# Kernel tuning notes

Measured on AMD Instinct MI355X. Metric: run time of the kernel, lower is better.

The kernel has to match this reference:

```python
import jax, jax.numpy as jnp
import numpy as np


def setup_inputs() -> dict:
    key = jax.random.key(0)
    ks = jax.random.split(key, 12)
    B, N, E = 8, 10000, 320000
    x = jax.random.normal(ks[0], (B, N, 3), dtype=jnp.float32)
    edge_index = jax.random.randint(ks[1], (2, E), 0, N, dtype=jnp.int64)
    # edge_attr: [dist, direction]; dist kept away from 0 to avoid div-by-zero
    dist = jax.random.uniform(ks[2], (E,), dtype=jnp.float32) * 9.0 + 1.0
    direc = jax.random.uniform(ks[3], (E,), dtype=jnp.float32) * 2.0 * np.pi
    edge_attr = jnp.stack([dist, direc], axis=-1)
    wind_mean = jax.random.uniform(ks[4], (2,), dtype=jnp.float32) * 2.0
    wind_std = jax.random.uniform(ks[5], (2,), dtype=jnp.float32) + 0.5
    s = lambda k, sh, fan: jax.random.normal(k, sh, dtype=jnp.float32) / np.sqrt(fan)
    W1 = s(ks[6], (9, 16), 9)
    b1 = jnp.zeros((16,), jnp.float32)
    W2 = s(ks[7], (16, 30), 16)
    b2 = jnp.zeros((30,), jnp.float32)
    W3 = s(ks[8], (30, 3), 30)
    b3 = jnp.zeros((3,), jnp.float32)
    return {"x": x, "edge_index": edge_index, "edge_attr": edge_attr,
            "wind_mean": wind_mean, "wind_std": wind_std,
            "W1": W1, "b1": b1, "W2": W2, "b2": b2, "W3": W3, "b3": b3}


def reference(x, edge_index, edge_attr, wind_mean, wind_std, W1, b1, W2, b2, W3, b3):
    B, N, _ = x.shape
    src, tgt = edge_index[0], edge_index[1]
    node_src = x[:, src]    # [B,E,3] gather
    node_tgt = x[:, tgt]    # [B,E,3]
    # denormalize wind (last 2 features of source node)
    src_wind = node_src[:, :, -2:] * wind_std[None, None, :] + wind_mean[None, None, :]
    speed = src_wind[:, :, 0]
    direc = src_wind[:, :, 1]
    city_dist = edge_attr[:, 0][None, :]   # [1,E]
    city_direc = edge_attr[:, 1][None, :]
    theta = jnp.abs(city_direc - direc)
    edge_weight = jax.nn.relu(3.0 * speed * jnp.cos(theta) / city_dist)  # [B,E]
    # normalize edge_attr (torch .std uses ddof=1)
    ea_norm = (edge_attr - edge_attr.mean(axis=0)) / edge_attr.std(axis=0, ddof=1)
    ea_norm_b = jnp.broadcast_to(ea_norm[None], (B,) + ea_norm.shape)
    feat = jnp.concatenate([node_src, node_tgt, ea_norm_b, edge_weight[:, :, None]], axis=-1)  # [B,E,9]
    h = jax.nn.sigmoid(feat @ W1 + b1)
    h = jax.nn.sigmoid(h @ W2 + b2)        # [B,E,30]
    agg = jnp.zeros((B, N, h.shape[-1]), h.dtype)
    agg = agg.at[:, tgt].add(h).at[:, src].add(-h)   # scatter_add + scatter_sub
    return jax.nn.sigmoid(agg @ W3 + b3)   # [B,N,3]
```

## Files before the change

kernel.cpp:

```cpp
#include <hip/hip_runtime.h>
#include <hip/hip_fp16.h>
#include <math.h>

#define BB 8
#define NB 128
#define NBINS 10016
#define FPAD 14

typedef float f32x2 __attribute__((ext_vector_type(2)));
typedef float f32x4 __attribute__((ext_vector_type(4)));
typedef _Float16 h16x4 __attribute__((ext_vector_type(4)));

__device__ __forceinline__ float sigmoidf_(float v) {
    return __builtin_amdgcn_rcpf(1.0f + __expf(-v));
}
__device__ __forceinline__ float sigs_(float d) {
    return __builtin_amdgcn_rcpf(1.0f + __builtin_amdgcn_exp2f(-d));
}
__device__ __forceinline__ unsigned pkh2_(float a, float b) {
    __half2 h = __floats2half2_rn(a, b);
    return *reinterpret_cast<unsigned*>(&h);
}

__global__ __launch_bounds__(256) void prep_kernel(
    const float* __restrict__ ea, const int* __restrict__ ei,
    const float* __restrict__ x, float* __restrict__ xT,
    unsigned short* __restrict__ cnt2, double* __restrict__ acc,
    int N, int E, int full)
{
    __shared__ unsigned hist[NBINS];
    __shared__ double sh[4][256];
    int tid = threadIdx.x;
    int blk = blockIdx.x;

    if (full) {
        for (int b = tid; b < NBINS; b += 256) hist[b] = 0u;
    }

    double s0 = 0, q0 = 0, s1 = 0, q1 = 0;
    for (int i = blk * 256 + tid; i < E; i += NB * 256) {
        float a = ea[2 * i];
        float b = ea[2 * i + 1];
        s0 += (double)a; q0 += (double)a * (double)a;
        s1 += (double)b; q1 += (double)b * (double)b;
    }

    if (full) {
        int xtotal = N * BB * 3;
        for (int idx = blk * 256 + tid; idx < xtotal; idx += NB * 256) {
            int c = idx % 3;
            int rest = idx / 3;
            int n = rest % N;
            int b = rest / N;
            xT[n * 24 + b * 3 + c] = x[idx];
        }
        __syncthreads();
        int chunk = (E + NB - 1) / NB;
        int s = blk * chunk;
        int epd = min(E, s + chunk);
        for (int e = s + tid; e < epd; e += 256) {
            atomicAdd(&hist[ei[E + e]], 1u);
            atomicAdd(&hist[ei[e]], 1u);
        }
        __syncthreads();
        unsigned short* row = cnt2 + (size_t)blk * NBINS;
        for (int b = tid; b < NBINS; b += 256)
            row[b] = (unsigned short)hist[b];
    }

    sh[0][tid] = s0; sh[1][tid] = q0; sh[2][tid] = s1; sh[3][tid] = q1;
    __syncthreads();
    for (int off = 128; off > 0; off >>= 1) {
        if (tid < off) {
            sh[0][tid] += sh[0][tid + off];
            sh[1][tid] += sh[1][tid + off];
            sh[2][tid] += sh[2][tid + off];
            sh[3][tid] += sh[3][tid + off];
        }
        __syncthreads();
    }
    if (tid == 0) {
        atomicAdd(&acc[0], sh[0][0]);
        atomicAdd(&acc[1], sh[1][0]);
        atomicAdd(&acc[2], sh[2][0]);
        atomicAdd(&acc[3], sh[3][0]);
    }
}

__global__ __launch_bounds__(256) void base_kernel(unsigned short* __restrict__ cnt2,
                                                   int* __restrict__ tot) {
    int bin = blockIdx.x * 256 + threadIdx.x;
    if (bin >= NBINS) return;
    unsigned run = 0;
    #pragma unroll 8
    for (int blk = 0; blk < NB; blk++) {
        size_t idx = (size_t)blk * NBINS + bin;
        unsigned v = cnt2[idx];
        cnt2[idx] = (unsigned short)run;
        run += v;
    }
    tot[bin] = (int)run;
}

__global__ __launch_bounds__(1024) void scan_kernel(const int* __restrict__ tot,
                                                    int* __restrict__ off, int N,
                                                    const double* __restrict__ acc, int E,
                                                    float* __restrict__ stats) {
    if (threadIdx.x == 0) {
        double s0 = acc[0], q0 = acc[1], s1 = acc[2], q1 = acc[3];
        double v0 = (q0 - s0 * s0 / E) / (double)(E - 1);
        double v1 = (q1 - s1 * s1 / E) / (double)(E - 1);
        stats[0] = (float)(s0 / E);
        stats[1] = (float)(1.0 / sqrt(v0));
        stats[2] = (float)(s1 / E);
        stats[3] = (float)(1.0 / sqrt(v1));
    }
    __shared__ int sh[1024];
    int t = threadIdx.x;
    int chunk = (N + 1023) >> 10;
    int lo = t * chunk;
    int hi = lo + chunk; if (hi > N) hi = N;
    int s = 0;
    for (int i = lo; i < hi; i++) s += tot[i];
    sh[t] = s;
    __syncthreads();
    for (int d = 1; d < 1024; d <<= 1) {
        int v = (t >= d) ? sh[t - d] : 0;
        __syncthreads();
        sh[t] += v;
        __syncthreads();
    }
    int run = (t == 0) ? 0 : sh[t - 1];
    for (int i = lo; i < hi; i++) {
        off[i] = run;
        run += tot[i];
    }
    if (t == 1023) off[N] = sh[1023];
}

__global__ __launch_bounds__(256) void ranklist_kernel(
    const int* __restrict__ ei, int E,
    const unsigned short* __restrict__ cnt2,
    const int* __restrict__ off, int* __restrict__ list)
{
    __shared__ unsigned hist[NBINS];
    int tid = threadIdx.x;
    int blk = blockIdx.x;
    for (int b = tid; b < NBINS; b += 256) hist[b] = 0u;
    __syncthreads();

    int chunk = (E + NB - 1) / NB;
    int s = blk * chunk;
    int epd = min(E, s + chunk);
    const unsigned short* row = cnt2 + (size_t)blk * NBINS;
    for (int e = s + tid; e < epd; e += 256) {
        int tgt = ei[E + e];
        int src = ei[e];
        unsigned lt = atomicAdd(&hist[tgt], 1u);
        unsigned ls = atomicAdd(&hist[src], 1u);
        list[off[tgt] + (int)row[tgt] + (int)lt] = e;
        list[off[src] + (int)row[src] + (int)ls] = e | 0x80000000;
    }
}

__global__ __launch_bounds__(256) void edge_mlp_mfma_kernel(
    const float* __restrict__ xT, const int* __restrict__ ei,
    const float* __restrict__ ea,
    const float* __restrict__ wmean, const float* __restrict__ wstd,
    const float* __restrict__ W1, const float* __restrict__ b1,
    const float* __restrict__ W2, const float* __restrict__ b2,
    const float* __restrict__ W3,
    const double* __restrict__ acc,
    uint2* __restrict__ gbuf,
    int N, int E)
{
    __shared__ unsigned fsh[4][64][FPAD];

    int lane = threadIdx.x & 63;
    int wave = threadIdx.x >> 6;
    int g = lane >> 4;
    int arow = lane & 15;

    const float LOG2E = 1.44269504088896340736f;

    double as0 = acc[0], aq0 = acc[1], as1 = acc[2], aq1 = acc[3];
    double v0 = (aq0 - as0 * as0 / E) / (double)(E - 1);
    double v1 = (aq1 - as1 * as1 / E) / (double)(E - 1);
    float st0 = (float)(as0 / E);
    float st1 = (float)(1.0 / sqrt(v0));
    float st2 = (float)(as1 / E);
    float st3 = (float)(1.0 / sqrt(v1));

    h16x4 A1, A2a, A2b, A3a, A3b;
    #pragma unroll
    for (int j = 0; j < 4; j++) {
        int k = 4 * g + j;
        A1[j]  = (_Float16)((k < 9) ? W1[k * 16 + arow] * LOG2E : 0.0f);
        A2a[j] = (_Float16)(W2[k * 30 + arow] * LOG2E);
        A2b[j] = (_Float16)((arow < 14) ? W2[k * 30 + 16 + arow] * LOG2E : 0.0f);
        A3a[j] = (_Float16)((arow < 3) ? W3[k * 3 + arow] : 0.0f);
        int k2 = 16 + k;
        A3b[j] = (_Float16)((arow < 3 && k2 < 30) ? W3[k2 * 3 + arow] : 0.0f);
    }
    f32x4 C1, C2a, C2b;
    #pragma unroll
    for (int r = 0; r < 4; r++) {
        int row = 4 * g + r;
        C1[r]  = b1[row] * LOG2E;
        C2a[r] = b2[row] * LOG2E;
        C2b[r] = (row < 14) ? b2[16 + row] * LOG2E : 0.0f;
    }

    float wm0 = wmean[0], wm1 = wmean[1];
    float wsd0 = wstd[0], wsd1 = wstd[1];

    int e_loc = lane >> 3;
    int bb = lane & 7;

    for (int grp = blockIdx.x; grp * 32 < E; grp += gridDim.x) {
        int ebase = grp * 32 + wave * 8;
        if (ebase >= E) continue;

        int e = ebase + e_loc;
        int esafe = (e < E) ? e : (E - 1);
        int src = ei[esafe];
        int tgt = ei[E + esafe];
        float dist = ea[2 * esafe];
        float cdir = ea[2 * esafe + 1];

        const float* xs = xT + src * 24 + bb * 3;
        const float* xt = xT + tgt * 24 + bb * 3;
        float s0 = xs[0], s1 = xs[1], s2 = xs[2];
        float t0 = xt[0], t1 = xt[1], t2 = xt[2];
        float ea0 = (dist - st0) * st1;
        float ea1 = (cdir - st2) * st3;
        float speed = fmaf(s1, wsd0, wm0);
        float direc = fmaf(s2, wsd1, wm1);
        float theta = fabsf(cdir - direc);
        float ew = fmaxf(0.0f, speed * __cosf(theta) * 3.0f * __builtin_amdgcn_rcpf(dist));

        unsigned* fp = &fsh[wave][lane][0];
        uint4 wv0, wv1;
        wv0.x = pkh2_(s0, s1); wv0.y = pkh2_(s2, t0);
        wv0.z = pkh2_(t1, t2); wv0.w = pkh2_(ea0, ea1);
        wv1.x = pkh2_(ew, 0.0f); wv1.y = 0u; wv1.z = 0u; wv1.w = 0u;
        *reinterpret_cast<uint4*>(fp) = wv0;
        *reinterpret_cast<uint4*>(fp + 4) = wv1;

        #pragma unroll
        for (int t = 0; t < 4; t++) {
            const unsigned* q = &fsh[wave][t * 16 + arow][0];
            union { uint2 u; h16x4 h; } b1u;
            b1u.u = *reinterpret_cast<const uint2*>(q + 2 * g);

            f32x4 D1 = __builtin_amdgcn_mfma_f32_16x16x16f16(A1, b1u.h, C1, 0, 0, 0);
            union { uint2 u; h16x4 h; } b2u;
            b2u.u.x = pkh2_(sigs_(D1[0]), sigs_(D1[1]));
            b2u.u.y = pkh2_(sigs_(D1[2]), sigs_(D1[3]));

            f32x4 D2a = __builtin_amdgcn_mfma_f32_16x16x16f16(A2a, b2u.h, C2a, 0, 0, 0);
            f32x4 D2b = __builtin_amdgcn_mfma_f32_16x16x16f16(A2b, b2u.h, C2b, 0, 0, 0);
            union { uint2 u; h16x4 h; } b3au, b3bu;
            b3au.u.x = pkh2_(sigs_(D2a[0]), sigs_(D2a[1]));
            b3au.u.y = pkh2_(sigs_(D2a[2]), sigs_(D2a[3]));
            b3bu.u.x = pkh2_(sigs_(D2b[0]), sigs_(D2b[1]));
            b3bu.u.y = pkh2_(sigs_(D2b[2]), sigs_(D2b[3]));

            f32x4 Z = {0.f, 0.f, 0.f, 0.f};
            f32x4 D3 = __builtin_amdgcn_mfma_f32_16x16x16f16(A3a, b3au.h, Z, 0, 0, 0);
            D3 = __builtin_amdgcn_mfma_f32_16x16x16f16(A3b, b3bu.h, D3, 0, 0, 0);

            if (g == 0) {
                int et = ebase + 2 * t + (arow >> 3);
                int bt = arow & 7;
                if (et < E) {
                    uint2 wp;
                    wp.x = pkh2_(D3[0], D3[1]);
                    wp.y = pkh2_(D3[2], 0.0f);
                    gbuf[(size_t)et * BB + bt] = wp;
                }
            }
        }
    }
}

__global__ __launch_bounds__(256) void node_sum_kernel(
    const uint2* __restrict__ gbuf, const int* __restrict__ off,
    const int* __restrict__ list,
    const float* __restrict__ b3, float* __restrict__ out, int N)
{
    int node = blockIdx.x * 4 + (threadIdx.x >> 6);
    int lane = threadIdx.x & 63;
    if (node >= N) return;

    int o0 = off[node], o1 = off[node + 1];
    float a[BB][3];
    #pragma unroll
    for (int b = 0; b < BB; b++) { a[b][0] = 0.f; a[b][1] = 0.f; a[b][2] = 0.f; }

    for (int i = o0 + lane; i < o1; i += 64) {
        int entry = list[i];
        int e = entry & 0x7FFFFFFF;
        float sgn = (entry < 0) ? -1.0f : 1.0f;
        const uint4* gl = reinterpret_cast<const uint4*>(gbuf + (size_t)e * BB);
        uint4 q0 = gl[0], q1 = gl[1], q2 = gl[2], q3 = gl[3];

        #define ACC_(bi, u01, u2x) {                                              \
            float2 f01 = __half22float2(*reinterpret_cast<const __half2*>(&u01)); \
            float2 f2  = __half22float2(*reinterpret_cast<const __half2*>(&u2x)); \
            a[bi][0] = fmaf(sgn, f01.x, a[bi][0]);                                \
            a[bi][1] = fmaf(sgn, f01.y, a[bi][1]);                                \
            a[bi][2] = fmaf(sgn, f2.x,  a[bi][2]); }
        ACC_(0, q0.x, q0.y) ACC_(1, q0.z, q0.w)
        ACC_(2, q1.x, q1.y) ACC_(3, q1.z, q1.w)
        ACC_(4, q2.x, q2.y) ACC_(5, q2.z, q2.w)
        ACC_(6, q3.x, q3.y) ACC_(7, q3.z, q3.w)
        #undef ACC_
    }

    #pragma unroll
    for (int m = 32; m >= 1; m >>= 1) {
        #pragma unroll
        for (int b = 0; b < BB; b++) {
            a[b][0] += __shfl_xor(a[b][0], m);
            a[b][1] += __shfl_xor(a[b][1], m);
            a[b][2] += __shfl_xor(a[b][2], m);
        }
    }

    float bb0 = b3[0], bb1 = b3[1], bb2 = b3[2];
    #pragma unroll
    for (int b = 0; b < BB; b++) {
        if (lane == b) {
            float* o = out + ((size_t)b * N + node) * 3;
            o[0] = sigmoidf_(a[b][0] + bb0);
            o[1] = sigmoidf_(a[b][1] + bb1);
            o[2] = sigmoidf_(a[b][2] + bb2);
        }
    }
}

__global__ void finalize_stats_kernel(const double* __restrict__ acc, int E,
                                      float* __restrict__ stats) {
    double s0 = acc[0], q0 = acc[1], s1 = acc[2], q1 = acc[3];
    double v0 = (q0 - s0 * s0 / E) / (double)(E - 1);
    double v1 = (q1 - s1 * s1 / E) / (double)(E - 1);
    stats[0] = (float)(s0 / E);
    stats[1] = (float)(1.0 / sqrt(v0));
    stats[2] = (float)(s1 / E);
    stats[3] = (float)(1.0 / sqrt(v1));
}

__device__ __forceinline__ void mlp_eval(
    const float feat[9],
    const float* __restrict__ W1, const float* __restrict__ b1,
    const float* __restrict__ W2, const float* __restrict__ b2,
    const float* __restrict__ W3,
    float& g0, float& g1, float& g2)
{
    const f32x2* W1p = (const f32x2*)W1;
    const f32x2* b1p = (const f32x2*)b1;
    f32x2 acc1[8];
    #pragma unroll
    for (int j = 0; j < 8; j++) acc1[j] = b1p[j];
    #pragma unroll
    for (int k = 0; k < 9; k++) {
        f32x2 fk2 = {feat[k], feat[k]};
        #pragma unroll
        for (int j = 0; j < 8; j++)
            acc1[j] = __builtin_elementwise_fma(fk2, W1p[k * 8 + j], acc1[j]);
    }
    float h1[16];
    #pragma unroll
    for (int j = 0; j < 8; j++) {
        h1[2 * j]     = sigmoidf_(acc1[j].x);
        h1[2 * j + 1] = sigmoidf_(acc1[j].y);
    }
    const f32x2* W2p = (const f32x2*)W2;
    const f32x2* b2p = (const f32x2*)b2;
    f32x2 acc2[15];
    #pragma unroll
    for (int k = 0; k < 15; k++) acc2[k] = b2p[k];
    #pragma unroll
    for (int j = 0; j < 16; j++) {
        f32x2 hj2 = {h1[j], h1[j]};
        #pragma unroll
        for (int k = 0; k < 15; k++)
            acc2[k] = __builtin_elementwise_fma(hj2, W2p[j * 15 + k], acc2[k]);
    }
    g0 = 0.f; g1 = 0.f; g2 = 0.f;
    #pragma unroll
    for (int k = 0; k < 15; k++) {
        float ha = sigmoidf_(acc2[k].x);
        float hb = sigmoidf_(acc2[k].y);
        int ka = 2 * k, kb = 2 * k + 1;
        g0 = fmaf(ha, W3[ka * 3 + 0], g0); g0 = fmaf(hb, W3[kb * 3 + 0], g0);
        g1 = fmaf(ha, W3[ka * 3 + 1], g1); g1 = fmaf(hb, W3[kb * 3 + 1], g1);
        g2 = fmaf(ha, W3[ka * 3 + 2], g2); g2 = fmaf(hb, W3[kb * 3 + 2], g2);
    }
}

__global__ __launch_bounds__(256) void edge_atomic_kernel(
    const float* __restrict__ x, const int* __restrict__ ei,
    const float* __restrict__ ea,
    const float* __restrict__ wmean, const float* __restrict__ wstd,
    const float* __restrict__ W1, const float* __restrict__ b1,
    const float* __restrict__ W2, const float* __restrict__ b2,
    const float* __restrict__ W3,
    const float* __restrict__ stats,
    float* __restrict__ out, int N, int E)
{
    int e = blockIdx.x * blockDim.x + threadIdx.x;
    if (e >= E) return;
    int src = ei[e];
    int tgt = ei[E + e];
    float dist = ea[2 * e];
    float cdir = ea[2 * e + 1];
    float ea0 = (dist - stats[0]) * stats[1];
    float ea1 = (cdir - stats[2]) * stats[3];

    for (int b = 0; b < BB; b++) {
        const float* xb = x + (size_t)b * N * 3;
        float s0 = xb[src * 3 + 0], s1 = xb[src * 3 + 1], s2 = xb[src * 3 + 2];
        float t0 = xb[tgt * 3 + 0], t1 = xb[tgt * 3 + 1], t2 = xb[tgt * 3 + 2];
        float speed = fmaf(s1, wstd[0], wmean[0]);
        float direc = fmaf(s2, wstd[1], wmean[1]);
        float theta = fabsf(cdir - direc);
        float ew = fmaxf(0.0f, speed * __cosf(theta) * 3.0f * __builtin_amdgcn_rcpf(dist));
        float feat[9] = {s0, s1, s2, t0, t1, t2, ea0, ea1, ew};
        float g0, g1, g2;
        mlp_eval(feat, W1, b1, W2, b2, W3, g0, g1, g2);
        float* ot = out + ((size_t)b * N + tgt) * 3;
        float* os = out + ((size_t)b * N + src) * 3;
        atomicAdd(&ot[0], g0);  atomicAdd(&ot[1], g1);  atomicAdd(&ot[2], g2);
        atomicAdd(&os[0], -g0); atomicAdd(&os[1], -g1); atomicAdd(&os[2], -g2);
    }
}

__global__ void output_kernel(float* __restrict__ out, const float* __restrict__ b3, int total) {
    int i = blockIdx.x * blockDim.x + threadIdx.x;
    if (i < total) out[i] = sigmoidf_(out[i] + b3[i % 3]);
}

extern "C" void kernel_launch(void* const* d_in, const int* in_sizes, int n_in,
                              void* d_out, int out_size, void* d_ws, size_t ws_size,
                              hipStream_t stream) {
    const float* x     = (const float*)d_in[0];
    const int*   ei    = (const int*)d_in[1];
    const float* ea    = (const float*)d_in[2];
    const float* wmean = (const float*)d_in[3];
    const float* wstd  = (const float*)d_in[4];
    const float* W1    = (const float*)d_in[5];
    const float* b1    = (const float*)d_in[6];
    const float* W2    = (const float*)d_in[7];
    const float* b2    = (const float*)d_in[8];
    const float* W3    = (const float*)d_in[9];
    const float* b3    = (const float*)d_in[10];

    int E = in_sizes[2] / 2;
    int N = in_sizes[0] / (BB * 3);

    float* out = (float*)d_out;
    char* ws = (char*)d_ws;

    double* acc   = (double*)ws;
    float*  stats = (float*)(ws + 32);
    int*    tot   = (int*)(ws + 64);
    int*    off   = tot + NBINS;
    int*    list  = off + N + 1;

    size_t xtOff = 64 + sizeof(int) * ((size_t)NBINS + (N + 1) + 2 * (size_t)E);
    xtOff = (xtOff + 255) & ~(size_t)255;
    float* xT = (float*)(ws + xtOff);

    size_t c2Off = xtOff + (size_t)N * 24 * sizeof(float);
    c2Off = (c2Off + 255) & ~(size_t)255;
    unsigned short* cnt2 = (unsigned short*)(ws + c2Off);

    size_t gbOff = c2Off + (size_t)NB * NBINS * sizeof(unsigned short);
    gbOff = (gbOff + 255) & ~(size_t)255;
    uint2* gbuf = (uint2*)(ws + gbOff);
    size_t needed = gbOff + (size_t)E * BB * sizeof(uint2);

    int eblocks = (E + 255) / 256;
    int fastPath = (needed <= ws_size && N <= NBINS) ? 1 : 0;

    hipMemsetAsync(acc, 0, 32, stream);

    if (fastPath) {
        prep_kernel<<<NB, 256, 0, stream>>>(ea, ei, x, xT, cnt2, acc, N, E, 1);
        base_kernel<<<(NBINS + 255) / 256, 256, 0, stream>>>(cnt2, tot);
        scan_kernel<<<1, 1024, 0, stream>>>(tot, off, N, acc, E, stats);
        ranklist_kernel<<<NB, 256, 0, stream>>>(ei, E, cnt2, off, list);
        int groups = (E + 31) / 32;
        int mblocks = (groups < 2048) ? groups : 2048;
        edge_mlp_mfma_kernel<<<mblocks, 256, 0, stream>>>(
            xT, ei, ea, wmean, wstd, W1, b1, W2, b2, W3, acc, gbuf, N, E);
        node_sum_kernel<<<(N + 3) / 4, 256, 0, stream>>>(
            gbuf, off, list, b3, out, N);
    } else {
        hipMemsetAsync(d_out, 0, (size_t)out_size * sizeof(float), stream);
        prep_kernel<<<NB, 256, 0, stream>>>(ea, ei, x, xT, cnt2, acc, N, E, 0);
        finalize_stats_kernel<<<1, 1, 0, stream>>>(acc, E, stats);
        edge_atomic_kernel<<<eblocks, 256, 0, stream>>>(
            x, ei, ea, wmean, wstd, W1, b1, W2, b2, W3, stats, out, N, E);
        output_kernel<<<(out_size + 255) / 256, 256, 0, stream>>>(out, b3, out_size);
    }
}
```

Baseline: 120.6 us.

## Fuse ranklist into edge MLP kernel and replace stats atomics with per-block partials

```diff
diff --git a/kernel.cpp b/kernel.cpp
--- a/kernel.cpp
+++ b/kernel.cpp
@@ -25,7 +25,7 @@
 __global__ __launch_bounds__(256) void prep_kernel(
     const float* __restrict__ ea, const int* __restrict__ ei,
     const float* __restrict__ x, float* __restrict__ xT,
-    unsigned short* __restrict__ cnt2, double* __restrict__ acc,
+    unsigned short* __restrict__ cnt2, double* __restrict__ accp,
     int N, int E, int full)
 {
     __shared__ unsigned hist[NBINS];
@@ -80,10 +80,10 @@
         __syncthreads();
     }
     if (tid == 0) {
-        atomicAdd(&acc[0], sh[0][0]);
-        atomicAdd(&acc[1], sh[1][0]);
-        atomicAdd(&acc[2], sh[2][0]);
-        atomicAdd(&acc[3], sh[3][0]);
+        accp[4 * blk + 0] = sh[0][0];
+        accp[4 * blk + 1] = sh[1][0];
+        accp[4 * blk + 2] = sh[2][0];
+        accp[4 * blk + 3] = sh[3][0];
     }
 }
 
@@ -104,10 +104,16 @@
 
 __global__ __launch_bounds__(1024) void scan_kernel(const int* __restrict__ tot,
                                                     int* __restrict__ off, int N,
-                                                    const double* __restrict__ acc, int E,
+                                                    const double* __restrict__ accp, int E,
                                                     float* __restrict__ stats) {
     if (threadIdx.x == 0) {
-        double s0 = acc[0], q0 = acc[1], s1 = acc[2], q1 = acc[3];
+        double s0 = 0, q0 = 0, s1 = 0, q1 = 0;
+        for (int b = 0; b < NB; b++) {
+            s0 += accp[4 * b + 0];
+            q0 += accp[4 * b + 1];
+            s1 += accp[4 * b + 2];
+            q1 += accp[4 * b + 3];
+        }
         double v0 = (q0 - s0 * s0 / E) / (double)(E - 1);
         double v1 = (q1 - s1 * s1 / E) / (double)(E - 1);
         stats[0] = (float)(s0 / E);
@@ -138,58 +144,55 @@
     if (t == 1023) off[N] = sh[1023];
 }
 
-__global__ __launch_bounds__(256) void ranklist_kernel(
-    const int* __restrict__ ei, int E,
-    const unsigned short* __restrict__ cnt2,
-    const int* __restrict__ off, int* __restrict__ list)
-{
-    __shared__ unsigned hist[NBINS];
-    int tid = threadIdx.x;
-    int blk = blockIdx.x;
-    for (int b = tid; b < NBINS; b += 256) hist[b] = 0u;
-    __syncthreads();
-
-    int chunk = (E + NB - 1) / NB;
-    int s = blk * chunk;
-    int epd = min(E, s + chunk);
-    const unsigned short* row = cnt2 + (size_t)blk * NBINS;
-    for (int e = s + tid; e < epd; e += 256) {
-        int tgt = ei[E + e];
-        int src = ei[e];
-        unsigned lt = atomicAdd(&hist[tgt], 1u);
-        unsigned ls = atomicAdd(&hist[src], 1u);
-        list[off[tgt] + (int)row[tgt] + (int)lt] = e;
-        list[off[src] + (int)row[src] + (int)ls] = e | 0x80000000;
-    }
-}
-
-__global__ __launch_bounds__(256) void edge_mlp_mfma_kernel(
+__global__ __launch_bounds__(256) void fused_rank_mlp_kernel(
     const float* __restrict__ xT, const int* __restrict__ ei,
     const float* __restrict__ ea,
     const float* __restrict__ wmean, const float* __restrict__ wstd,
     const float* __restrict__ W1, const float* __restrict__ b1,
     const float* __restrict__ W2, const float* __restrict__ b2,
     const float* __restrict__ W3,
-    const double* __restrict__ acc,
+    const float* __restrict__ stats,
+    const unsigned short* __restrict__ cnt2,
+    const int* __restrict__ off, int* __restrict__ list,
     uint2* __restrict__ gbuf,
     int N, int E)
 {
-    __shared__ unsigned fsh[4][64][FPAD];
-
-    int lane = threadIdx.x & 63;
-    int wave = threadIdx.x >> 6;
+    __shared__ unsigned smem[NBINS];
+    int tid = threadIdx.x;
+
+    if (blockIdx.x < NB) {
+        unsigned* hist = smem;
+        int blk = blockIdx.x;
+        for (int b = tid; b < NBINS; b += 256) hist[b] = 0u;
+        __syncthreads();
+        int chunk = (E + NB - 1) / NB;
+        int s = blk * chunk;
+        int epd = min(E, s + chunk);
+        const unsigned short* row = cnt2 + (size_t)blk * NBINS;
+        for (int e = s + tid; e < epd; e += 256) {
+            int tgt = ei[E + e];
+            int src = ei[e];
+            unsigned lt = atomicAdd(&hist[tgt], 1u);
+            unsigned ls = atomicAdd(&hist[src], 1u);
+            list[off[tgt] + (int)row[tgt] + (int)lt] = e;
+            list[off[src] + (int)row[src] + (int)ls] = e | 0x80000000;
+        }
+        return;
+    }
+
+    typedef unsigned fsh_t[64][FPAD];
+    fsh_t* fsh = reinterpret_cast<fsh_t*>(smem);
+
+    int mlp_id = blockIdx.x - NB;
+    int nmlp = gridDim.x - NB;
+    int lane = tid & 63;
+    int wave = tid >> 6;
     int g = lane >> 4;
     int arow = lane & 15;
 
     const float LOG2E = 1.44269504088896340736f;
 
-    double as0 = acc[0], aq0 = acc[1], as1 = acc[2], aq1 = acc[3];
-    double v0 = (aq0 - as0 * as0 / E) / (double)(E - 1);
-    double v1 = (aq1 - as1 * as1 / E) / (double)(E - 1);
-    float st0 = (float)(as0 / E);
-    float st1 = (float)(1.0 / sqrt(v0));
-    float st2 = (float)(as1 / E);
-    float st3 = (float)(1.0 / sqrt(v1));
+    float st0 = stats[0], st1 = stats[1], st2 = stats[2], st3 = stats[3];
 
     h16x4 A1, A2a, A2b, A3a, A3b;
     #pragma unroll
@@ -217,7 +220,7 @@
     int e_loc = lane >> 3;
     int bb = lane & 7;
 
-    for (int grp = blockIdx.x; grp * 32 < E; grp += gridDim.x) {
+    for (int grp = mlp_id; grp * 32 < E; grp += nmlp) {
         int ebase = grp * 32 + wave * 8;
         if (ebase >= E) continue;
 
@@ -340,9 +343,15 @@
     }
 }
 
-__global__ void finalize_stats_kernel(const double* __restrict__ acc, int E,
+__global__ void finalize_stats_kernel(const double* __restrict__ accp, int E,
                                       float* __restrict__ stats) {
-    double s0 = acc[0], q0 = acc[1], s1 = acc[2], q1 = acc[3];
+    double s0 = 0, q0 = 0, s1 = 0, q1 = 0;
+    for (int b = 0; b < NB; b++) {
+        s0 += accp[4 * b + 0];
+        q0 += accp[4 * b + 1];
+        s1 += accp[4 * b + 2];
+        q1 += accp[4 * b + 3];
+    }
     double v0 = (q0 - s0 * s0 / E) / (double)(E - 1);
     double v1 = (q1 - s1 * s1 / E) / (double)(E - 1);
     stats[0] = (float)(s0 / E);
@@ -463,13 +472,14 @@
     float* out = (float*)d_out;
     char* ws = (char*)d_ws;
 
-    double* acc   = (double*)ws;
-    float*  stats = (float*)(ws + 32);
-    int*    tot   = (int*)(ws + 64);
+    double* accp  = (double*)ws;
+    float*  stats = (float*)(ws + NB * 4 * sizeof(double));
+    int*    tot   = (int*)(ws + NB * 4 * sizeof(double) + 64);
     int*    off   = tot + NBINS;
     int*    list  = off + N + 1;
 
-    size_t xtOff = 64 + sizeof(int) * ((size_t)NBINS + (N + 1) + 2 * (size_t)E);
+    size_t xtOff = NB * 4 * sizeof(double) + 64 +
+                   sizeof(int) * ((size_t)NBINS + (N + 1) + 2 * (size_t)E);
     xtOff = (xtOff + 255) & ~(size_t)255;
     float* xT = (float*)(ws + xtOff);
 
@@ -485,23 +495,19 @@
     int eblocks = (E + 255) / 256;
     int fastPath = (needed <= ws_size && N <= NBINS) ? 1 : 0;
 
-    hipMemsetAsync(acc, 0, 32, stream);
-
     if (fastPath) {
-        prep_kernel<<<NB, 256, 0, stream>>>(ea, ei, x, xT, cnt2, acc, N, E, 1);
+        prep_kernel<<<NB, 256, 0, stream>>>(ea, ei, x, xT, cnt2, accp, N, E, 1);
         base_kernel<<<(NBINS + 255) / 256, 256, 0, stream>>>(cnt2, tot);
-        scan_kernel<<<1, 1024, 0, stream>>>(tot, off, N, acc, E, stats);
-        ranklist_kernel<<<NB, 256, 0, stream>>>(ei, E, cnt2, off, list);
-        int groups = (E + 31) / 32;
-        int mblocks = (groups < 2048) ? groups : 2048;
-        edge_mlp_mfma_kernel<<<mblocks, 256, 0, stream>>>(
-            xT, ei, ea, wmean, wstd, W1, b1, W2, b2, W3, acc, gbuf, N, E);
+        scan_kernel<<<1, 1024, 0, stream>>>(tot, off, N, accp, E, stats);
+        fused_rank_mlp_kernel<<<NB + 1920, 256, 0, stream>>>(
+            xT, ei, ea, wmean, wstd, W1, b1, W2, b2, W3, stats,
+            cnt2, off, list, gbuf, N, E);
         node_sum_kernel<<<(N + 3) / 4, 256, 0, stream>>>(
             gbuf, off, list, b3, out, N);
     } else {
         hipMemsetAsync(d_out, 0, (size_t)out_size * sizeof(float), stream);
-        prep_kernel<<<NB, 256, 0, stream>>>(ea, ei, x, xT, cnt2, acc, N, E, 0);
-        finalize_stats_kernel<<<1, 1, 0, stream>>>(acc, E, stats);
+        prep_kernel<<<NB, 256, 0, stream>>>(ea, ei, x, xT, cnt2, accp, N, E, 0);
+        finalize_stats_kernel<<<1, 1, 0, stream>>>(accp, E, stats);
         edge_atomic_kernel<<<eblocks, 256, 0, stream>>>(
             x, ei, ea, wmean, wstd, W1, b1, W2, b2, W3, stats, out, N, E);
         output_kernel<<<(out_size + 255) / 256, 256, 0, stream>>>(out, b3, out_size);
```

Result: faster. 108.6 us (-9.9%).
